# Optimization experiments

Measured on AMD Instinct MI355X. Metric: run time of the kernel, lower is better.

## Reference

```python
import jax, jax.numpy as jnp
import numpy as np

DIM = 1024
HEADS = 16
HEAD_DIM = DIM // HEADS
T_MAX = 128
V = 12
T = 128
B = 4
N = V * T + 1  # 1537, includes cls token


def setup_inputs() -> dict:
    key = jax.random.key(0)
    ks = jax.random.split(key, 9)
    s = 0.02
    return {
        "x": jax.random.normal(ks[0], (B, N, DIM), dtype=jnp.float32),
        "qkv_w": jax.random.normal(ks[1], (3 * DIM, DIM), dtype=jnp.float32) * s,
        "in_proj_w": jax.random.normal(ks[2], (3 * DIM, DIM), dtype=jnp.float32) * s,
        "in_proj_b": jax.random.normal(ks[3], (3 * DIM,), dtype=jnp.float32) * s,
        "out_proj_w": jax.random.normal(ks[4], (DIM, DIM), dtype=jnp.float32) * s,
        "out_proj_b": jax.random.normal(ks[5], (DIM,), dtype=jnp.float32) * s,
        "proj_w": jax.random.normal(ks[6], (DIM, DIM), dtype=jnp.float32) * s,
        "proj_b": jax.random.normal(ks[7], (DIM,), dtype=jnp.float32) * s,
        "ids_restore": jax.random.randint(ks[8], (B, V * T), 0, 1000000, dtype=jnp.int64),
        "V_input": V,
        "T_input": T,
    }


def _rope_tables(dtype):
    # theta_d = 10000^{-2d/head_dim}, positions 0..T_max (position 0 is the cls slot)
    theta = 10000.0 ** (-jnp.arange(0, HEAD_DIM, 2, dtype=dtype) / HEAD_DIM)  # (hd/2,)
    pos = jnp.arange(1 + T_MAX, dtype=dtype)
    ang = pos[:, None] * theta[None, :]  # (1+T_max, hd/2)
    return jnp.cos(ang), jnp.sin(ang)


def _rotate(t, cos_g, sin_g):
    # t: (B, N, D); cos_g/sin_g: (B, N-1, 1, hd/2) gathered per non-cls token
    b, n, d = t.shape
    t4 = t.reshape(b, n, HEADS, HEAD_DIM)
    re, im = t4[..., ::2], t4[..., 1::2]  # even/odd interleave -> (B,N,H,hd/2)
    # cls token uses position 0: cos=1, sin=0 -> identity rotation, halves concatenated
    cls = jnp.concatenate([re[:, :1], im[:, :1]], axis=-1)  # (B,1,H,hd)
    rest = jnp.concatenate(
        [re[:, 1:] * cos_g - im[:, 1:] * sin_g,
         re[:, 1:] * sin_g + im[:, 1:] * cos_g], axis=-1)  # (B,N-1,H,hd)
    return jnp.concatenate([cls, rest], axis=1).reshape(b, n, d)


def reference(x, qkv_w, in_proj_w, in_proj_b, out_proj_w, out_proj_b,
              proj_w, proj_b, ids_restore, V_input, T_input):
    b, n, d = x.shape
    # --- qkv projection (no bias) ---
    qkv = jnp.einsum('bnd,ed->bne', x, qkv_w)  # (B,N,3D)
    q, k, v = jnp.split(qkv, 3, axis=-1)
    # --- temporal RoPE with ids_restore-based gather ---
    cos_t, sin_t = _rope_tables(x.dtype)  # (1+T_max, hd/2)
    ids_shuffle = jnp.argsort(ids_restore, axis=1)[:, : n - 1] % V_input  # (B,N-1)
    cos_g = cos_t[ids_shuffle + 1][:, :, None, :]  # gather from cos[:,1:] slice
    sin_g = sin_t[ids_shuffle + 1][:, :, None, :]
    q = _rotate(q, cos_g, sin_g)
    k = _rotate(k, cos_g, sin_g)
    # --- nn.MultiheadAttention (batch_first, no mask, eval) ---
    wq, wk, wv = in_proj_w[:d], in_proj_w[d:2 * d], in_proj_w[2 * d:]
    bq, bk, bv = in_proj_b[:d], in_proj_b[d:2 * d], in_proj_b[2 * d:]
    qp = (jnp.einsum('bnd,ed->bne', q, wq) + bq).reshape(b, n, HEADS, HEAD_DIM)
    kp = (jnp.einsum('bnd,ed->bne', k, wk) + bk).reshape(b, n, HEADS, HEAD_DIM)
    vp = (jnp.einsum('bnd,ed->bne', v, wv) + bv).reshape(b, n, HEADS, HEAD_DIM)
    scale = 1.0 / jnp.sqrt(jnp.asarray(HEAD_DIM, x.dtype))
    scores = jnp.einsum('bqhe,bkhe->bhqk', qp * scale, kp)  # (B,H,N,N)
    attn = jax.nn.softmax(scores, axis=-1)
    ctx = jnp.einsum('bhqk,bkhe->bqhe', attn, vp).reshape(b, n, d)
    mha_out = jnp.einsum('bnd,ed->bne', ctx, out_proj_w) + out_proj_b
    # --- final projection ---
    out = jnp.einsum('bnd,ed->bne', mha_out, proj_w) + proj_b
    return out


if __name__ == '__main__':
    inp = setup_inputs()
    print(reference(**inp).shape)
```

## Files before the change

kernel.cpp:

```cpp
#include <hip/hip_runtime.h>
#include <math.h>

#define B_ 4
#define NTOK 1537
#define NH 16
#define NROWS 6148
#define RPAD 6272
#define KDIM 1024
#define NKT 49

typedef __attribute__((ext_vector_type(8))) short short8;
typedef __attribute__((ext_vector_type(4))) float f32x4;
typedef __attribute__((ext_vector_type(16))) float f32x16;
typedef __attribute__((ext_vector_type(4))) unsigned short ushort4v;
typedef __attribute__((ext_vector_type(4))) unsigned int uint4v;
typedef __attribute__((ext_vector_type(2))) unsigned int uint2v;

__device__ __forceinline__ float bf2f(unsigned short u){
  unsigned int x = ((unsigned int)u) << 16;
  return __uint_as_float(x);
}
__device__ __forceinline__ unsigned short f2bf(float f){
  unsigned int x = __float_as_uint(f);
  x += 0x7fff + ((x >> 16) & 1);
  return (unsigned short)(x >> 16);
}
__device__ __forceinline__ unsigned int pack_bf16(float lo, float hi){
  return (unsigned int)f2bf(lo) | ((unsigned int)f2bf(hi) << 16);
}
__device__ __forceinline__ unsigned int pack_bf16_fast(float lo, float hi){
  unsigned int ue = __float_as_uint(lo) + 0x8000u;
  unsigned int uo = __float_as_uint(hi) + 0x8000u;
  return __builtin_amdgcn_perm(uo, ue, 0x07060302u);
}
__device__ __forceinline__ float fast_exp2(float x){
  return __builtin_amdgcn_exp2f(x);
}
__device__ __forceinline__ uint2v permswap(unsigned int a, unsigned int b){
  return __builtin_amdgcn_permlane32_swap(a, b, false, false);
}
__device__ __forceinline__ void gload_lds16(const void* g, void* l){
  __builtin_amdgcn_global_load_lds((const __attribute__((address_space(1))) unsigned int*)g,
                                   (__attribute__((address_space(3))) unsigned int*)l, 16, 0, 0);
}
__device__ __forceinline__ f32x4 mfma16(short8 a, short8 b, f32x4 c){
  return __builtin_amdgcn_mfma_f32_16x16x32_bf16(a, b, c, 0, 0, 0);
}
__device__ __forceinline__ f32x16 mfma32(short8 a, short8 b, f32x16 c){
  return __builtin_amdgcn_mfma_f32_32x32x16_bf16(a, b, c, 0, 0, 0);
}
__device__ __forceinline__ void xcd_swz(int nx, int ny, int& bx, int& by){
  int lin = blockIdx.y * nx + blockIdx.x;
  int cpx = (nx * ny) >> 3;
  int swz = (lin & 7) * cpx + (lin >> 3);
  bx = swz % nx;
  by = swz / nx;
}

__global__ __launch_bounds__(256) void cvt_w_kernel(const float* __restrict__ src,
                                                    unsigned short* __restrict__ dst, int n){
  int i = (blockIdx.x*256 + threadIdx.x)*4;
  if (i >= n) return;
  f32x4 v = *(const f32x4*)(src + i);
  ushort4v o;
  #pragma unroll
  for (int j=0;j<4;j++) o[j] = f2bf(v[j]);
  *(ushort4v*)(dst + i) = o;
}

__global__ __launch_bounds__(256) void cvt_wT_kernel(const float* __restrict__ src, int r0,
                                                     unsigned short* __restrict__ dst){
  __shared__ float Tl[64][65];
  int ct = blockIdx.x, rt = blockIdx.y;
  int t = threadIdx.x;
  int i = t >> 4, j4 = (t & 15) * 4;
  #pragma unroll
  for (int s = 0; s < 4; s++){
    int rl = s*16 + i;
    f32x4 v = *(const f32x4*)(src + (size_t)(r0 + rt*64 + rl)*1024 + ct*64 + j4);
    Tl[rl][j4+0]=v[0]; Tl[rl][j4+1]=v[1]; Tl[rl][j4+2]=v[2]; Tl[rl][j4+3]=v[3];
  }
  __syncthreads();
  #pragma unroll
  for (int s = 0; s < 4; s++){
    int cl = s*16 + i;
    ushort4v o;
    #pragma unroll
    for (int k=0;k<4;k++) o[k] = f2bf(Tl[j4+k][cl]);
    *(ushort4v*)(dst + (size_t)(ct*64 + cl)*1024 + rt*64 + j4) = o;
  }
}

__global__ __launch_bounds__(256) void cvt_x_kernel(const float* __restrict__ x,
                                                    unsigned short* __restrict__ xb){
  size_t i = ((size_t)blockIdx.x*256 + threadIdx.x)*4;
  if (i >= (size_t)RPAD*KDIM) return;
  size_t row = i >> 10;
  ushort4v o;
  if (row < NROWS){
    f32x4 v = *(const f32x4*)(x + i);
    #pragma unroll
    for (int j=0;j<4;j++) o[j] = f2bf(v[j]);
  } else {
    o = (ushort4v)0;
  }
  *(ushort4v*)(xb + i) = o;
}

__global__ __launch_bounds__(64) void fuse_bias_kernel(const float* __restrict__ pw,
    const float* __restrict__ opb, const float* __restrict__ pb, float* __restrict__ bf){
  int c = blockIdx.x;
  int t = threadIdx.x;
  const float* row = pw + (size_t)c*1024;
  float s = 0.f;
  #pragma unroll
  for (int e=0; e<16; e++) s += row[t + e*64] * opb[t + e*64];
  #pragma unroll
  for (int off=1; off<64; off<<=1) s += __shfl_xor(s, off);
  if (t == 0) bf[c] = s + pb[c];
}

__global__ void rope_tables_kernel(float* __restrict__ ct, float* __restrict__ st){
  int i = threadIdx.x;
  if (i >= 13*32) return;
  int p = i >> 5, j = i & 31;
  float th = powf(10000.f, -(float)j * (1.f/32.f));
  float ang = (float)p * th;
  ct[i] = cosf(ang);
  st[i] = sinf(ang);
}

__global__ __launch_bounds__(256) void argsort_kernel(const int* __restrict__ ids,
                                                      int* __restrict__ postab){
  __shared__ int vals[1536];
  int b = blockIdx.x;
  const int* src = ids + b*1536;
  for (int i=threadIdx.x; i<1536; i+=256) vals[i] = src[i];
  __syncthreads();
  int i = blockIdx.y*256 + threadIdx.x;
  int v = vals[i];
  int rank = 0;
  for (int j=0;j<1536;j++){
    int u = vals[j];
    rank += (u < v) || (u == v && j < i);
  }
  postab[b*1536 + rank] = (i % 12) + 1;
}

__global__ __launch_bounds__(256) void rope_kernel(unsigned short* __restrict__ qkv,
                                                   const int* __restrict__ postab,
                                                   const float* __restrict__ ct,
                                                   const float* __restrict__ st){
  int idx = blockIdx.x*256 + threadIdx.x;
  if (idx >= B_*NTOK*NH) return;
  int h = idx & 15;
  int bn = idx >> 4;
  int b = bn / NTOK;
  int n = bn - b*NTOK;
  unsigned short* rowp = qkv + (size_t)bn*2048;
  int pos = (n == 0) ? 0 : postab[b*1536 + (n-1)];
  const float* cr = ct + pos*32;
  const float* sr = st + pos*32;
  #pragma unroll
  for (int part=0; part<2; part++){
    unsigned short* p = rowp + part*1024 + h*64;
    uint4v vv[8];
    #pragma unroll
    for (int i=0;i<8;i++) vv[i] = ((const uint4v*)p)[i];
    unsigned short* tp = (unsigned short*)vv;
    unsigned short ov[64];
    if (n == 0){
      #pragma unroll
      for (int j=0;j<32;j++){ ov[j] = tp[2*j]; ov[32+j] = tp[2*j+1]; }
    } else {
      #pragma unroll
      for (int j=0;j<32;j++){
        float re = bf2f(tp[2*j]), im = bf2f(tp[2*j+1]);
        float c = cr[j], s = sr[j];
        ov[j]    = f2bf(re*c - im*s);
        ov[32+j] = f2bf(re*s + im*c);
      }
    }
    #pragma unroll
    for (int i=0;i<8;i++) ((uint4v*)p)[i] = ((const uint4v*)ov)[i];
  }
}

__device__ __forceinline__ void gemm_body(const unsigned short* __restrict__ A, int lda,
    const unsigned short* __restrict__ W,
    const float* __restrict__ bias, float scale,
    unsigned short* __restrict__ outb, float* __restrict__ outf, int ldo, int mvalid,
    int rowBase, int colBase)
{
  __shared__ alignas(16) unsigned short At[128][32];
  __shared__ alignas(16) unsigned short Bt[128][32];
  int t = threadIdx.x, w = t >> 6, lane = t & 63;
  int g = lane >> 4, l15 = lane & 15;
  int rb = (w >> 1) * 64, cb = (w & 1) * 64;
  f32x4 acc[4][4];
  #pragma unroll
  for (int m=0;m<4;m++)
    #pragma unroll
    for (int n=0;n<4;n++) acc[m][n] = 0.f;
  int srow = lane >> 2;
  int scol = ((lane & 3) ^ ((lane >> 3) & 3)) * 8;
  int rc   = (g ^ ((l15 >> 1) & 3)) * 8;
  for (int kb = 0; kb < KDIM; kb += 32){
    __syncthreads();
    #pragma unroll
    for (int i=0;i<2;i++){
      int rr = i*64 + w*16 + srow;
      gload_lds16(A + (size_t)(rowBase + rr)*lda + kb + scol, &At[i*64 + w*16][0]);
      gload_lds16(W + (size_t)(colBase + rr)*KDIM + kb + scol, &Bt[i*64 + w*16][0]);
    }
    __syncthreads();
    short8 af[4], bf[4];
    #pragma unroll
    for (int m=0;m<4;m++) af[m] = *(const short8*)&At[rb + m*16 + l15][rc];
    #pragma unroll
    for (int n=0;n<4;n++) bf[n] = *(const short8*)&Bt[cb + n*16 + l15][rc];
    #pragma unroll
    for (int m=0;m<4;m++)
      #pragma unroll
      for (int n=0;n<4;n++)
        acc[m][n] = mfma16(af[m], bf[n], acc[m][n]);
  }
  #pragma unroll
  for (int m=0;m<4;m++)
    #pragma unroll
    for (int n=0;n<4;n++){
      int col = colBase + cb + n*16 + l15;
      float bv = bias ? bias[col] : 0.f;
      #pragma unroll
      for (int r=0;r<4;r++){
        int row = rowBase + rb + m*16 + g*4 + r;
        if (row < mvalid){
          float v = (acc[m][n][r] + bv) * scale;
          if (outf) outf[(size_t)row*ldo + col] = v;
          else      outb[(size_t)row*ldo + col] = f2bf(v);
        }
      }
    }
}

__global__ __launch_bounds__(256) void gemm_kernel(const unsigned short* __restrict__ A, int lda,
    const unsigned short* __restrict__ W,
    const float* __restrict__ bias, float scale,
    unsigned short* __restrict__ outb, float* __restrict__ outf, int ldo, int mvalid)
{
  int bx, by; xcd_swz(RPAD/128, 8, bx, by);
  gemm_body(A, lda, W, bias, scale, outb, outf, ldo, mvalid, bx*128, by*128);
}

__global__ __launch_bounds__(256) void gemm_qkv_kernel(const unsigned short* __restrict__ xb,
    const unsigned short* __restrict__ qkvwb, const unsigned short* __restrict__ Wvb,
    const float* __restrict__ ipb, unsigned short* __restrict__ qkb,
    unsigned short* __restrict__ vpb)
{
  int bx, by; xcd_swz(RPAD/128, 24, bx, by);
  bool isV = by >= 16;
  const unsigned short* W = isV ? Wvb : qkvwb;
  const float* bias = isV ? ipb + 2048 : nullptr;
  unsigned short* outb = isV ? vpb : qkb;
  int ldo = isV ? 1024 : 2048;
  int colBase = (isV ? by - 16 : by) * 128;
  gemm_body(xb, 1024, W, bias, 1.f, outb, nullptr, ldo, NROWS, bx*128, colBase);
}

__global__ __launch_bounds__(256) void gemm_inproj_kernel(const unsigned short* __restrict__ qkb,
    const unsigned short* __restrict__ ipwb, const float* __restrict__ ipb,
    unsigned short* __restrict__ qpb, unsigned short* __restrict__ kpb)
{
  int z = blockIdx.z;
  int bx, by; xcd_swz(RPAD/128, 8, bx, by);
  const unsigned short* A = qkb + z*1024;
  const unsigned short* W = ipwb + (size_t)z*1024*1024;
  const float* bias = ipb + z*1024;
  float scale = (z == 0) ? 0.125f*1.44269504f : 1.f;
  unsigned short* outb = (z == 0) ? qpb : kpb;
  gemm_body(A, 2048, W, bias, scale, outb, nullptr, 1024, NROWS, bx*128, by*128);
}

__global__ __launch_bounds__(256) void gemm_prep_kernel(const unsigned short* __restrict__ pwb,
    const unsigned short* __restrict__ opwT, const unsigned short* __restrict__ wv,
    const unsigned short* __restrict__ qkvwTv,
    unsigned short* __restrict__ Wfb, unsigned short* __restrict__ Wvb)
{
  int z = blockIdx.z;
  const unsigned short* A = z ? wv : pwb;
  const unsigned short* W = z ? qkvwTv : opwT;
  unsigned short* outb = z ? Wvb : Wfb;
  gemm_body(A, 1024, W, nullptr, 1.f, outb, nullptr, 1024, 1024,
            blockIdx.x*128, blockIdx.y*128);
}

__global__ __launch_bounds__(256) void frag_kernel(const unsigned short* __restrict__ kp,
    const unsigned short* __restrict__ vp,
    unsigned short* __restrict__ kf, unsigned short* __restrict__ vf){
  __shared__ alignas(16) unsigned short Tl[32][72];
  int bh = blockIdx.x, kt = blockIdx.y;
  int b = bh >> 4, h = bh & 15;
  int t = threadIdx.x;
  if (blockIdx.z == 0){
    int lane = t & 63, c = t >> 6;
    int l31 = lane & 31, hh = lane >> 5;
    int key = kt*32 + l31; if (key > NTOK-1) key = NTOK-1;
    uint4v v = *(const uint4v*)(kp + (size_t)(b*NTOK + key)*KDIM + h*64 + c*16 + hh*8);
    *(uint4v*)(kf + (size_t)(bh*NKT + kt)*2048 + c*512 + lane*8) = v;
  } else {
    {
      int r = t >> 3, ch = t & 7;
      int key = kt*32 + r;
      uint4v v;
      if (key < NTOK){
        v = *(const uint4v*)(vp + (size_t)(b*NTOK + key)*KDIM + h*64 + ch*8);
      } else v = (uint4v)0;
      *(uint4v*)&Tl[r][ch*8] = v;
    }
    __syncthreads();
    {
      int lane = t & 63, w = t >> 6;
      int l31 = lane & 31, hh = lane >> 5;
      int dblk = w >> 1, c = w & 1;
      unsigned short ov[8];
      #pragma unroll
      for (int j=0;j<8;j++) ov[j] = Tl[c*16 + hh*8 + j][dblk*32 + l31];
      *(uint4v*)(vf + (size_t)(bh*NKT + kt)*2048 + w*512 + lane*8) = *(const uint4v*)ov;
    }
  }
}

__global__ __launch_bounds__(256) void attn_kernel(const unsigned short* __restrict__ qp,
    const unsigned short* __restrict__ kf, const unsigned short* __restrict__ vf,
    unsigned short* __restrict__ ctx)
{
  int bh = blockIdx.x;
  int qt = blockIdx.y;
  int b = bh >> 4, hd = bh & 15;
  int t = threadIdx.x, w = t >> 6, lane = t & 63;
  int l31 = lane & 31, hh = lane >> 5;
  int qrow = qt*128 + w*32 + l31;
  int qcl = qrow > NTOK-1 ? NTOK-1 : qrow;
  const unsigned short* qb = qp + (((size_t)(b*NTOK + qcl)*NH + hd) << 6) + hh*8;
  short8 qf[4];
  #pragma unroll
  for (int c=0;c<4;c++) qf[c] = *(const short8*)(qb + c*16);
  const unsigned short* kfb = kf + (size_t)(bh*NKT)*2048 + lane*8;
  const unsigned short* vfb = vf + (size_t)(bh*NKT)*2048 + lane*8;
  float m_ = -3e38f, l_ = 0.f;
  f32x16 o0 = 0.f, o1 = 0.f;

  auto soft_pv = [&](f32x16 cc, short8 va00, short8 va01, short8 va10, short8 va11){
    float t0 = fmaxf(fmaxf(cc[0],cc[1]), fmaxf(cc[2],cc[3]));
    float t1 = fmaxf(fmaxf(cc[4],cc[5]), fmaxf(cc[6],cc[7]));
    float t2 = fmaxf(fmaxf(cc[8],cc[9]), fmaxf(cc[10],cc[11]));
    float t3 = fmaxf(fmaxf(cc[12],cc[13]), fmaxf(cc[14],cc[15]));
    float mx = fmaxf(fmaxf(t0,t1), fmaxf(t2,t3));
    {
      uint2v pr = permswap(__float_as_uint(mx), __float_as_uint(mx));
      mx = fmaxf(__uint_as_float(pr[0]), __uint_as_float(pr[1]));
    }
    if (!__all(mx <= m_ + 11.5f)){
      float mn = fmaxf(m_, mx);
      float al = fast_exp2(m_ - mn);
      m_ = mn;
      l_ *= al;
      #pragma unroll
      for (int i=0;i<16;i++){ o0[i] *= al; o1[i] *= al; }
    }
    float p[16], rs = 0.f;
    #pragma unroll
    for (int i=0;i<16;i++){ p[i] = fast_exp2(cc[i] - m_); }
    #pragma unroll
    for (int i=0;i<16;i++) rs += p[i];
    l_ += rs;
    unsigned int W[8];
    #pragma unroll
    for (int wd=0; wd<8; wd++) W[wd] = pack_bf16_fast(p[2*wd], p[2*wd+1]);
    uint2v e0 = permswap(W[0], W[2]);
    uint2v e1 = permswap(W[1], W[3]);
    uint2v e2 = permswap(W[4], W[6]);
    uint2v e3 = permswap(W[5], W[7]);
    uint4v u0, u1;
    u0[0]=e0[0]; u0[1]=e1[0]; u0[2]=e0[1]; u0[3]=e1[1];
    u1[0]=e2[0]; u1[1]=e3[0]; u1[2]=e2[1]; u1[3]=e3[1];
    short8 pb0, pb1;
    __builtin_memcpy(&pb0, &u0, 16);
    __builtin_memcpy(&pb1, &u1, 16);
    o0 = mfma32(va00, pb0, o0);
    o0 = mfma32(va01, pb1, o0);
    o1 = mfma32(va10, pb0, o1);
    o1 = mfma32(va11, pb1, o1);
  };

  short8 ka[4];
  #pragma unroll
  for (int c=0;c<4;c++) ka[c] = *(const short8*)(kfb + c*512);
  f32x16 cc = 0.f;
  cc = mfma32(ka[0], qf[0], cc);
  cc = mfma32(ka[1], qf[1], cc);
  cc = mfma32(ka[2], qf[2], cc);
  cc = mfma32(ka[3], qf[3], cc);
  #pragma unroll
  for (int c=0;c<4;c++) ka[c] = *(const short8*)(kfb + 2048 + c*512);

  for (int kt=0; kt<48; ++kt){
    const unsigned short* vB = vfb + (size_t)kt*2048;
    short8 va00 = *(const short8*)(vB);
    short8 va01 = *(const short8*)(vB + 512);
    short8 va10 = *(const short8*)(vB + 1024);
    short8 va11 = *(const short8*)(vB + 1536);
    f32x16 cn = 0.f;
    cn = mfma32(ka[0], qf[0], cn);
    cn = mfma32(ka[1], qf[1], cn);
    cn = mfma32(ka[2], qf[2], cn);
    cn = mfma32(ka[3], qf[3], cn);
    int ktn = kt+2 < NKT-1 ? kt+2 : NKT-1;
    const unsigned short* kB = kfb + (size_t)ktn*2048;
    #pragma unroll
    for (int c=0;c<4;c++) ka[c] = *(const short8*)(kB + c*512);
    soft_pv(cc, va00, va01, va10, va11);
    cc = cn;
  }
  {
    const unsigned short* vB = vfb + (size_t)48*2048;
    short8 va00 = *(const short8*)(vB);
    short8 va01 = *(const short8*)(vB + 512);
    short8 va10 = *(const short8*)(vB + 1024);
    short8 va11 = *(const short8*)(vB + 1536);
    #pragma unroll
    for (int i=0;i<16;i++) cc[i] = (i == 0 && hh == 0) ? cc[i] : -1e30f;
    soft_pv(cc, va00, va01, va10, va11);
  }
  {
    uint2v pr = permswap(__float_as_uint(l_), __float_as_uint(l_));
    l_ = __uint_as_float(pr[0]) + __uint_as_float(pr[1]);
  }
  if (qrow < NTOK){
    float inv = 1.f / l_;
    unsigned short* cb = ctx + (((size_t)(b*NTOK + qrow)*NH + hd) << 6) + 4*hh;
    #pragma unroll
    for (int s=0;s<4;s++){
      uint2v u;
      u[0] = pack_bf16(o0[4*s]*inv,   o0[4*s+1]*inv);
      u[1] = pack_bf16(o0[4*s+2]*inv, o0[4*s+3]*inv);
      *(uint2v*)(cb + 8*s) = u;
    }
    #pragma unroll
    for (int s=0;s<4;s++){
      uint2v u;
      u[0] = pack_bf16(o1[4*s]*inv,   o1[4*s+1]*inv);
      u[1] = pack_bf16(o1[4*s+2]*inv, o1[4*s+3]*inv);
      *(uint2v*)(cb + 32 + 8*s) = u;
    }
  }
}

extern "C" void kernel_launch(void* const* d_in, const int* in_sizes, int n_in,
                              void* d_out, int out_size, void* d_ws, size_t ws_size,
                              hipStream_t stream)
{
  const float* x    = (const float*)d_in[0];
  const float* qkvw = (const float*)d_in[1];
  const float* ipw  = (const float*)d_in[2];
  const float* ipb  = (const float*)d_in[3];
  const float* opw  = (const float*)d_in[4];
  const float* opb  = (const float*)d_in[5];
  const float* pw   = (const float*)d_in[6];
  const float* pb   = (const float*)d_in[7];
  const int*   ids  = (const int*)d_in[8];
  float* out = (float*)d_out;

  char* p = (char*)d_ws;
  auto alloc = [&](size_t bytes)->char* {
    char* r = p; p += (bytes + 255) & ~(size_t)255; return r;
  };
  unsigned short* xb     = (unsigned short*)alloc((size_t)RPAD*1024*2);
  unsigned short* qkvwb  = (unsigned short*)alloc((size_t)2048*1024*2);
  unsigned short* ipwb   = (unsigned short*)alloc((size_t)3072*1024*2);
  unsigned short* pwb    = (unsigned short*)alloc((size_t)1024*1024*2);
  unsigned short* opwT   = (unsigned short*)alloc((size_t)1024*1024*2);
  unsigned short* qkvwTv = (unsigned short*)alloc((size_t)1024*1024*2);
  unsigned short* Wfb    = (unsigned short*)alloc((size_t)1024*1024*2);
  unsigned short* Wvb    = (unsigned short*)alloc((size_t)1024*1024*2);
  float*          bfb    = (float*)alloc(1024*4);
  unsigned short* qkb    = (unsigned short*)alloc((size_t)RPAD*2048*2);
  unsigned short* qpb    = (unsigned short*)alloc((size_t)RPAD*1024*2);
  unsigned short* kpb    = (unsigned short*)alloc((size_t)RPAD*1024*2);
  unsigned short* vpb    = (unsigned short*)alloc((size_t)RPAD*1024*2);
  unsigned short* ctxb   = (unsigned short*)alloc((size_t)RPAD*1024*2);
  int*   postab = (int*)alloc((size_t)B_*1536*4);
  float* ctab   = (float*)alloc(13*32*4);
  float* stab   = (float*)alloc(13*32*4);
  unsigned short* vfb = xb;
  unsigned short* kfb = qkb;

  cvt_w_kernel<<<2048, 256, 0, stream>>>(qkvw, qkvwb, 2048*1024);
  cvt_w_kernel<<<3072, 256, 0, stream>>>(ipw,  ipwb,  3072*1024);
  cvt_w_kernel<<<1024, 256, 0, stream>>>(pw,   pwb,   1024*1024);
  cvt_wT_kernel<<<dim3(16,16), 256, 0, stream>>>(opw,  0,    opwT);
  cvt_wT_kernel<<<dim3(16,16), 256, 0, stream>>>(qkvw, 2048, qkvwTv);
  cvt_x_kernel<<<RPAD, 256, 0, stream>>>(x, xb);
  rope_tables_kernel<<<1, 512, 0, stream>>>(ctab, stab);
  argsort_kernel<<<dim3(B_, 6), 256, 0, stream>>>(ids, postab);

  gemm_prep_kernel<<<dim3(8, 8, 2), 256, 0, stream>>>(pwb, opwT, ipwb + (size_t)2048*1024,
                                                      qkvwTv, Wfb, Wvb);
  fuse_bias_kernel<<<1024, 64, 0, stream>>>(pw, opb, pb, bfb);

  gemm_qkv_kernel<<<dim3(RPAD/128, 24), 256, 0, stream>>>(xb, qkvwb, Wvb, ipb, qkb, vpb);
  rope_kernel<<<(B_*NTOK*NH + 255)/256, 256, 0, stream>>>(qkb, postab, ctab, stab);
  gemm_inproj_kernel<<<dim3(RPAD/128, 8, 2), 256, 0, stream>>>(qkb, ipwb, ipb, qpb, kpb);
  frag_kernel<<<dim3(B_*NH, NKT, 2), 256, 0, stream>>>(kpb, vpb, kfb, vfb);
  attn_kernel<<<dim3(B_*NH, 13), 256, 0, stream>>>(qpb, kfb, vfb, ctxb);
  gemm_kernel<<<dim3(RPAD/128, 8), 256, 0, stream>>>(ctxb, 1024, Wfb, bfb, 1.f,
                                                     nullptr, out, 1024, NROWS);
}
```

Measured before the change: 357.6 us.

## Fuse K fragment layout into in-proj GEMM epilogue and shrink attention blocks

The K in-projection GEMM now writes its output straight into the fragment layout the attention kernel consumes, so K no longer needs a separate pass to rearrange it. The frag kernel becomes V-only. Attention launches one 64-thread wave per 32-query tile instead of four waves per 128 queries, which increases block count from 832 to 3136. The tradeoffs are scattered 2-byte stores in the GEMM epilogue, and the loss of any sharing of K/V loads across waves in a block.

Measured after the change: 351.9 us. About the same (-1.6%).

```diff
diff --git a/kernel.cpp b/kernel.cpp
--- a/kernel.cpp
+++ b/kernel.cpp
@@ -190,7 +190,7 @@
     const unsigned short* __restrict__ W,
     const float* __restrict__ bias, float scale,
     unsigned short* __restrict__ outb, float* __restrict__ outf, int ldo, int mvalid,
-    int rowBase, int colBase)
+    int rowBase, int colBase, unsigned short* __restrict__ kfdst)
 {
   __shared__ alignas(16) unsigned short At[128][32];
   __shared__ alignas(16) unsigned short Bt[128][32];
@@ -224,6 +224,29 @@
       #pragma unroll
       for (int n=0;n<4;n++)
         acc[m][n] = mfma16(af[m], bf[n], acc[m][n]);
+  }
+  if (kfdst){
+    #pragma unroll
+    for (int m=0;m<4;m++)
+      #pragma unroll
+      for (int n=0;n<4;n++){
+        int col = colBase + cb + n*16 + l15;
+        float bv = bias[col];
+        int h  = col >> 6;
+        int c  = (col >> 4) & 3, hhd = (col >> 3) & 1, j = col & 7;
+        #pragma unroll
+        for (int r=0;r<4;r++){
+          int row = rowBase + rb + m*16 + g*4 + r;
+          if (row < mvalid){
+            int b  = row / NTOK;
+            int n_ = row - b*NTOK;
+            size_t off = ((size_t)((b*16 + h)*NKT + (n_ >> 5)))*2048
+                       + c*512 + hhd*256 + (n_ & 31)*8 + j;
+            kfdst[off] = f2bf(acc[m][n][r] + bv);
+          }
+        }
+      }
+    return;
   }
   #pragma unroll
   for (int m=0;m<4;m++)
@@ -249,7 +272,7 @@
     unsigned short* __restrict__ outb, float* __restrict__ outf, int ldo, int mvalid)
 {
   int bx, by; xcd_swz(RPAD/128, 8, bx, by);
-  gemm_body(A, lda, W, bias, scale, outb, outf, ldo, mvalid, bx*128, by*128);
+  gemm_body(A, lda, W, bias, scale, outb, outf, ldo, mvalid, bx*128, by*128, nullptr);
 }
 
 __global__ __launch_bounds__(256) void gemm_qkv_kernel(const unsigned short* __restrict__ xb,
@@ -264,21 +287,24 @@
   unsigned short* outb = isV ? vpb : qkb;
   int ldo = isV ? 1024 : 2048;
   int colBase = (isV ? by - 16 : by) * 128;
-  gemm_body(xb, 1024, W, bias, 1.f, outb, nullptr, ldo, NROWS, bx*128, colBase);
+  gemm_body(xb, 1024, W, bias, 1.f, outb, nullptr, ldo, NROWS, bx*128, colBase, nullptr);
 }
 
 __global__ __launch_bounds__(256) void gemm_inproj_kernel(const unsigned short* __restrict__ qkb,
     const unsigned short* __restrict__ ipwb, const float* __restrict__ ipb,
-    unsigned short* __restrict__ qpb, unsigned short* __restrict__ kpb)
+    unsigned short* __restrict__ qpb, unsigned short* __restrict__ kfb)
 {
   int z = blockIdx.z;
   int bx, by; xcd_swz(RPAD/128, 8, bx, by);
   const unsigned short* A = qkb + z*1024;
   const unsigned short* W = ipwb + (size_t)z*1024*1024;
   const float* bias = ipb + z*1024;
-  float scale = (z == 0) ? 0.125f*1.44269504f : 1.f;
-  unsigned short* outb = (z == 0) ? qpb : kpb;
-  gemm_body(A, 2048, W, bias, scale, outb, nullptr, 1024, NROWS, bx*128, by*128);
+  if (z == 0)
+    gemm_body(A, 2048, W, bias, 0.125f*1.44269504f, qpb, nullptr, 1024, NROWS,
+              bx*128, by*128, nullptr);
+  else
+    gemm_body(A, 2048, W, bias, 1.f, nullptr, nullptr, 0, NROWS,
+              bx*128, by*128, kfb);
 }
 
 __global__ __launch_bounds__(256) void gemm_prep_kernel(const unsigned short* __restrict__ pwb,
@@ -291,55 +317,46 @@
   const unsigned short* W = z ? qkvwTv : opwT;
   unsigned short* outb = z ? Wvb : Wfb;
   gemm_body(A, 1024, W, nullptr, 1.f, outb, nullptr, 1024, 1024,
-            blockIdx.x*128, blockIdx.y*128);
-}
-
-__global__ __launch_bounds__(256) void frag_kernel(const unsigned short* __restrict__ kp,
-    const unsigned short* __restrict__ vp,
-    unsigned short* __restrict__ kf, unsigned short* __restrict__ vf){
+            blockIdx.x*128, blockIdx.y*128, nullptr);
+}
+
+__global__ __launch_bounds__(256) void vfrag_kernel(const unsigned short* __restrict__ vp,
+                                                    unsigned short* __restrict__ vf){
   __shared__ alignas(16) unsigned short Tl[32][72];
   int bh = blockIdx.x, kt = blockIdx.y;
   int b = bh >> 4, h = bh & 15;
   int t = threadIdx.x;
-  if (blockIdx.z == 0){
-    int lane = t & 63, c = t >> 6;
+  {
+    int r = t >> 3, ch = t & 7;
+    int key = kt*32 + r;
+    uint4v v;
+    if (key < NTOK){
+      v = *(const uint4v*)(vp + (size_t)(b*NTOK + key)*KDIM + h*64 + ch*8);
+    } else v = (uint4v)0;
+    *(uint4v*)&Tl[r][ch*8] = v;
+  }
+  __syncthreads();
+  {
+    int lane = t & 63, w = t >> 6;
     int l31 = lane & 31, hh = lane >> 5;
-    int key = kt*32 + l31; if (key > NTOK-1) key = NTOK-1;
-    uint4v v = *(const uint4v*)(kp + (size_t)(b*NTOK + key)*KDIM + h*64 + c*16 + hh*8);
-    *(uint4v*)(kf + (size_t)(bh*NKT + kt)*2048 + c*512 + lane*8) = v;
-  } else {
-    {
-      int r = t >> 3, ch = t & 7;
-      int key = kt*32 + r;
-      uint4v v;
-      if (key < NTOK){
-        v = *(const uint4v*)(vp + (size_t)(b*NTOK + key)*KDIM + h*64 + ch*8);
-      } else v = (uint4v)0;
-      *(uint4v*)&Tl[r][ch*8] = v;
-    }
-    __syncthreads();
-    {
-      int lane = t & 63, w = t >> 6;
-      int l31 = lane & 31, hh = lane >> 5;
-      int dblk = w >> 1, c = w & 1;
-      unsigned short ov[8];
-      #pragma unroll
-      for (int j=0;j<8;j++) ov[j] = Tl[c*16 + hh*8 + j][dblk*32 + l31];
-      *(uint4v*)(vf + (size_t)(bh*NKT + kt)*2048 + w*512 + lane*8) = *(const uint4v*)ov;
-    }
-  }
-}
-
-__global__ __launch_bounds__(256) void attn_kernel(const unsigned short* __restrict__ qp,
+    int dblk = w >> 1, c = w & 1;
+    unsigned short ov[8];
+    #pragma unroll
+    for (int j=0;j<8;j++) ov[j] = Tl[c*16 + hh*8 + j][dblk*32 + l31];
+    *(uint4v*)(vf + (size_t)(bh*NKT + kt)*2048 + w*512 + lane*8) = *(const uint4v*)ov;
+  }
+}
+
+__global__ __launch_bounds__(64) void attn_kernel(const unsigned short* __restrict__ qp,
     const unsigned short* __restrict__ kf, const unsigned short* __restrict__ vf,
     unsigned short* __restrict__ ctx)
 {
   int bh = blockIdx.x;
   int qt = blockIdx.y;
   int b = bh >> 4, hd = bh & 15;
-  int t = threadIdx.x, w = t >> 6, lane = t & 63;
+  int lane = threadIdx.x;
   int l31 = lane & 31, hh = lane >> 5;
-  int qrow = qt*128 + w*32 + l31;
+  int qrow = qt*32 + l31;
   int qcl = qrow > NTOK-1 ? NTOK-1 : qrow;
   const unsigned short* qb = qp + (((size_t)(b*NTOK + qcl)*NH + hd) << 6) + hh*8;
   short8 qf[4];
@@ -486,14 +503,13 @@
   float*          bfb    = (float*)alloc(1024*4);
   unsigned short* qkb    = (unsigned short*)alloc((size_t)RPAD*2048*2);
   unsigned short* qpb    = (unsigned short*)alloc((size_t)RPAD*1024*2);
-  unsigned short* kpb    = (unsigned short*)alloc((size_t)RPAD*1024*2);
+  unsigned short* kfb    = (unsigned short*)alloc((size_t)64*NKT*2048*2);
   unsigned short* vpb    = (unsigned short*)alloc((size_t)RPAD*1024*2);
   unsigned short* ctxb   = (unsigned short*)alloc((size_t)RPAD*1024*2);
   int*   postab = (int*)alloc((size_t)B_*1536*4);
   float* ctab   = (float*)alloc(13*32*4);
   float* stab   = (float*)alloc(13*32*4);
   unsigned short* vfb = xb;
-  unsigned short* kfb = qkb;
 
   cvt_w_kernel<<<2048, 256, 0, stream>>>(qkvw, qkvwb, 2048*1024);
   cvt_w_kernel<<<3072, 256, 0, stream>>>(ipw,  ipwb,  3072*1024);
@@ -510,9 +526,9 @@
 
   gemm_qkv_kernel<<<dim3(RPAD/128, 24), 256, 0, stream>>>(xb, qkvwb, Wvb, ipb, qkb, vpb);
   rope_kernel<<<(B_*NTOK*NH + 255)/256, 256, 0, stream>>>(qkb, postab, ctab, stab);
-  gemm_inproj_kernel<<<dim3(RPAD/128, 8, 2), 256, 0, stream>>>(qkb, ipwb, ipb, qpb, kpb);
-  frag_kernel<<<dim3(B_*NH, NKT, 2), 256, 0, stream>>>(kpb, vpb, kfb, vfb);
-  attn_kernel<<<dim3(B_*NH, 13), 256, 0, stream>>>(qpb, kfb, vfb, ctxb);
+  gemm_inproj_kernel<<<dim3(RPAD/128, 8, 2), 256, 0, stream>>>(qkb, ipwb, ipb, qpb, kfb);
+  vfrag_kernel<<<dim3(B_*NH, NKT), 256, 0, stream>>>(vpb, vfb);
+  attn_kernel<<<dim3(B_*NH, NKT), 64, 0, stream>>>(qpb, kfb, vfb, ctxb);
   gemm_kernel<<<dim3(RPAD/128, 8), 256, 0, stream>>>(ctxb, 1024, Wfb, bfb, 1.f,
                                                      nullptr, out, 1024, NROWS);
 }
```
